# Optimization experiments

Measured on AMD Instinct MI355X. Metric: run time of the kernel, lower is better.

The kernel has to match this reference:

```python
import jax, jax.numpy as jnp
import numpy as np

N = 50000          # nodes
E = 800000         # edges (before self loops)
G = 64             # graphs in batch
HEADS = 4
HID = 25
DENSE = HEADS * HID      # 100, must equal prototype feature dim
IN_DIM = 128
OUT_DIM = 2
NPC = 5                  # num_prototypes_per_class
NUM_PROT = OUT_DIM * NPC
EPS = 1e-4
NEG_SLOPE = 0.2


def setup_inputs() -> dict:
    key = jax.random.key(0)
    ks = jax.random.split(key, 20)
    x = jax.random.normal(ks[0], (N, IN_DIM), dtype=jnp.float32)
    edge_index = jax.random.randint(ks[1], (2, E), 0, N, dtype=jnp.int64)
    batch = jnp.sort(jax.random.randint(ks[2], (N,), 0, G, dtype=jnp.int64))
    inp = {"x": x, "edge_index": edge_index, "batch": batch}
    in_dims = [IN_DIM, DENSE, DENSE]
    for i in range(3):
        d = in_dims[i]
        s = 1.0 / np.sqrt(d)
        inp[f"W{i}"] = jax.random.uniform(ks[3 + 4 * i], (d, DENSE), jnp.float32, -s, s)
        inp[f"as{i}"] = jax.random.uniform(ks[4 + 4 * i], (HEADS, HID), jnp.float32, -s, s)
        inp[f"ad{i}"] = jax.random.uniform(ks[5 + 4 * i], (HEADS, HID), jnp.float32, -s, s)
        inp[f"b{i}"] = jnp.zeros((DENSE,), jnp.float32)
    inp["protos"] = jax.random.uniform(ks[16], (NUM_PROT, DENSE), jnp.float32)
    # last_layer weight: +1 for own class, -0.5 otherwise  [OUT_DIM, NUM_PROT]
    cls = jnp.arange(NUM_PROT) // NPC
    inp["last_w"] = jnp.where(cls[None, :] == jnp.arange(OUT_DIM)[:, None], 1.0, -0.5).astype(jnp.float32)
    return inp


def _gat_layer(x, src, dst, W, a_src, a_dst, b):
    h = (x @ W).reshape(N, HEADS, HID)                 # [N,H,D]
    e_src = jnp.einsum('nhd,hd->nh', h, a_src)         # [N,H]
    e_dst = jnp.einsum('nhd,hd->nh', h, a_dst)
    alpha = e_src[src] + e_dst[dst]                    # [Etot,H]
    alpha = jnp.where(alpha > 0, alpha, NEG_SLOPE * alpha)
    amax = jax.ops.segment_max(alpha, dst, num_segments=N)
    ex = jnp.exp(alpha - amax[dst])
    denom = jax.ops.segment_sum(ex, dst, num_segments=N)
    a = ex / (denom[dst] + 1e-16)                      # segmented softmax over in-edges
    msg = h[src] * a[:, :, None]                       # [Etot,H,D]
    out = jax.ops.segment_sum(msg, dst, num_segments=N)
    return out.reshape(N, DENSE) + b


def reference(x, edge_index, batch, W0, as0, ad0, b0, W1, as1, ad1, b1, W2, as2, ad2, b2, protos, last_w):
    loops = jnp.arange(N, dtype=edge_index.dtype)
    src = jnp.concatenate([edge_index[0], loops])      # PyG add_self_loops=True
    dst = jnp.concatenate([edge_index[1], loops])
    params = [(W0, as0, ad0, b0), (W1, as1, ad1, b1), (W2, as2, ad2, b2)]
    h = x
    for (W, a_s, a_d, b) in params:
        h = _gat_layer(h, src, dst, W, a_s, a_d, b)
        h = jax.nn.relu(h)
    node_emb = h
    graph_emb = jax.ops.segment_max(h, batch, num_segments=G)   # global_max_pool
    # prototype distances: squared euclidean via expansion
    xp = graph_emb @ protos.T                                    # [G,P]
    dist = -2.0 * xp + jnp.sum(graph_emb ** 2, axis=1, keepdims=True) + jnp.sum(protos ** 2, axis=1)[None, :]
    sim = jnp.log((dist + 1.0) / (dist + EPS))
    logits = sim @ last_w.T
    probs = jax.nn.softmax(logits, axis=-1)
    return logits, probs, node_emb, graph_emb, dist
```

## Files before the change

kernel.cpp:

```cpp
#include <hip/hip_runtime.h>
#include <hip/hip_bf16.h>

#define NN      50000
#define EE      800000
#define ETOT    (EE + NN)
#define GG      64
#define HEADS   4
#define HID     25
#define DENSE   100
#define IN_DIM  128
#define OUT_DIM 2
#define NPC     5
#define NUM_PROT (OUT_DIM * NPC)
#define NCHUNK  ((NN + 255) / 256)

#define NEG_INF (-3.402823466e38f)

__global__ void k_count(const int* __restrict__ ei, int* __restrict__ cnt, int* __restrict__ pos) {
    int e = blockIdx.x * blockDim.x + threadIdx.x;
    if (e >= ETOT) return;
    int dst = (e < EE) ? ei[EE + e] : (e - EE);
    pos[e] = atomicAdd(&cnt[dst], 1);
}

__global__ void k_scan1(const int* __restrict__ cnt, int* __restrict__ csum) {
    __shared__ int sh[256];
    int i = blockIdx.x * 256 + threadIdx.x;
    int v = (i < NN) ? cnt[i] : 0;
    sh[threadIdx.x] = v;
    __syncthreads();
    for (int s = 128; s > 0; s >>= 1) {
        if (threadIdx.x < s) sh[threadIdx.x] += sh[threadIdx.x + s];
        __syncthreads();
    }
    if (threadIdx.x == 0) csum[blockIdx.x] = sh[0];
}

__global__ void k_scan2(int* __restrict__ csum) {
    __shared__ int sh[256];
    int tid = threadIdx.x;
    int v = (tid < NCHUNK) ? csum[tid] : 0;
    sh[tid] = v;
    __syncthreads();
    for (int s = 1; s < 256; s <<= 1) {
        int t = (tid >= s) ? sh[tid - s] : 0;
        __syncthreads();
        sh[tid] += t;
        __syncthreads();
    }
    if (tid < NCHUNK) csum[tid] = sh[tid] - v;
    if (tid == NCHUNK) csum[NCHUNK] = sh[255];
}

__global__ void k_scan3(const int* __restrict__ cnt, const int* __restrict__ csum, int* __restrict__ offs) {
    __shared__ int sh[256];
    int i = blockIdx.x * 256 + threadIdx.x;
    int v = (i < NN) ? cnt[i] : 0;
    sh[threadIdx.x] = v;
    __syncthreads();
    for (int s = 1; s < 256; s <<= 1) {
        int t = (threadIdx.x >= s) ? sh[threadIdx.x - s] : 0;
        __syncthreads();
        sh[threadIdx.x] += t;
        __syncthreads();
    }
    int excl = sh[threadIdx.x] - v + csum[blockIdx.x];
    if (i <= NN) offs[i] = excl;
}

__global__ void k_scatter(const int* __restrict__ ei, const int* __restrict__ offs,
                          const int* __restrict__ pos, int* __restrict__ csr) {
    int e = blockIdx.x * blockDim.x + threadIdx.x;
    if (e >= ETOT) return;
    int src, dst;
    if (e < EE) { src = ei[e]; dst = ei[EE + e]; }
    else        { src = dst = e - EE; }
    csr[offs[dst] + pos[e]] = src;
}

__global__ void k_bounds(const int* __restrict__ batch, int* __restrict__ gstart) {
    int n = blockIdx.x * blockDim.x + threadIdx.x;
    if (n >= NN) return;
    int b = batch[n];
    if (n == 0) {
        for (int g = 0; g <= b; g++) gstart[g] = 0;
    } else {
        int pb = batch[n - 1];
        for (int g = pb + 1; g <= b; g++) gstart[g] = n;
    }
    if (n == NN - 1) {
        for (int g = b + 1; g <= GG; g++) gstart[g] = NN;
    }
}

template <int DIN, int KC>
__global__ __launch_bounds__(256) void k_gemm(const float* __restrict__ X,
                                              const float* __restrict__ W,
                                              float* __restrict__ H) {
    constexpr int XSTR = KC + 4;
    __shared__ float Ws[KC * 104];
    __shared__ float Xs[128 * XSTR];
    const int tid = threadIdx.x;
    const int rl = tid >> 5;
    const int cg = tid & 31;
    const int node0 = blockIdx.x * 128;

    float acc[16][4] = {};
    constexpr int NCH = DIN / KC;
    constexpr int KQ = KC / 4;
    for (int kb = 0; kb < NCH; ++kb) {
        const int k0 = kb * KC;
        for (int idx = tid; idx < KC * 100; idx += 256) {
            int k = idx / 100, c = idx - k * 100;
            Ws[k * 104 + c] = W[(k0 + k) * 100 + c];
        }
        for (int q = tid; q < 128 * KQ; q += 256) {
            int r = q / KQ, kq = q - r * KQ;
            int row = node0 + r;
            float4 v = {0.f, 0.f, 0.f, 0.f};
            if (row < NN) v = *reinterpret_cast<const float4*>(&X[(size_t)row * DIN + k0 + kq * 4]);
            *reinterpret_cast<float4*>(&Xs[r * XSTR + kq * 4]) = v;
        }
        __syncthreads();
        if (cg < 25) {
            for (int kq = 0; kq < KQ; ++kq) {
                float4 w0 = *reinterpret_cast<const float4*>(&Ws[(kq * 4 + 0) * 104 + cg * 4]);
                float4 w1 = *reinterpret_cast<const float4*>(&Ws[(kq * 4 + 1) * 104 + cg * 4]);
                float4 w2 = *reinterpret_cast<const float4*>(&Ws[(kq * 4 + 2) * 104 + cg * 4]);
                float4 w3 = *reinterpret_cast<const float4*>(&Ws[(kq * 4 + 3) * 104 + cg * 4]);
                #pragma unroll
                for (int j = 0; j < 16; ++j) {
                    float4 xv = *reinterpret_cast<const float4*>(&Xs[(rl * 16 + j) * XSTR + kq * 4]);
                    acc[j][0] += xv.x * w0.x; acc[j][1] += xv.x * w0.y;
                    acc[j][2] += xv.x * w0.z; acc[j][3] += xv.x * w0.w;
                    acc[j][0] += xv.y * w1.x; acc[j][1] += xv.y * w1.y;
                    acc[j][2] += xv.y * w1.z; acc[j][3] += xv.y * w1.w;
                    acc[j][0] += xv.z * w2.x; acc[j][1] += xv.z * w2.y;
                    acc[j][2] += xv.z * w2.z; acc[j][3] += xv.z * w2.w;
                    acc[j][0] += xv.w * w3.x; acc[j][1] += xv.w * w3.y;
                    acc[j][2] += xv.w * w3.z; acc[j][3] += xv.w * w3.w;
                }
            }
        }
        __syncthreads();
    }
    if (cg < 25) {
        #pragma unroll
        for (int j = 0; j < 16; ++j) {
            int row = node0 + rl * 16 + j;
            if (row < NN) {
                float4 v = {acc[j][0], acc[j][1], acc[j][2], acc[j][3]};
                *reinterpret_cast<float4*>(&H[(size_t)row * 100 + cg * 4]) = v;
            }
        }
    }
}

__global__ void k_esed(const float* __restrict__ H, const float* __restrict__ AS,
                       const float* __restrict__ AD, float* __restrict__ es, float* __restrict__ ed) {
    int t = blockIdx.x * blockDim.x + threadIdx.x;
    if (t >= NN * HEADS) return;
    int n = t >> 2, hd = t & 3;
    const float* hr = H + (size_t)n * 100 + hd * 25;
    const float* as = AS + hd * 25;
    const float* ad = AD + hd * 25;
    float s1 = 0.f, s2 = 0.f;
    #pragma unroll
    for (int d = 0; d < 25; d++) {
        float v = hr[d];
        s1 += v * as[d];
        s2 += v * ad[d];
    }
    es[t] = s1;
    ed[t] = s2;
}

__global__ __launch_bounds__(256) void k_msum(const float* __restrict__ es,
                                              const float* __restrict__ ed,
                                              const int* __restrict__ offs,
                                              const int* __restrict__ csr,
                                              float* __restrict__ wv) {
    int wid = threadIdx.x >> 6;
    int lane = threadIdx.x & 63;
    int n = blockIdx.x * 4 + wid;
    if (n >= NN) return;
    int el = lane >> 2, hd = lane & 3;
    int beg = offs[n], end = offs[n + 1];
    float edh = ed[n * 4 + hd];
    float m = NEG_INF, s = 0.f;
    for (int e = beg + el; e < end; e += 16) {
        int si = csr[e];
        float a = es[si * 4 + hd] + edh;
        a = (a > 0.f) ? a : 0.2f * a;
        float nm = fmaxf(m, a);
        float sc = __expf(m - nm);
        s = s * sc + __expf(a - nm);
        m = nm;
    }
    #pragma unroll
    for (int mask = 4; mask <= 32; mask <<= 1) {
        float mo = __shfl_xor(m, mask, 64);
        float so = __shfl_xor(s, mask, 64);
        float nm = fmaxf(m, mo);
        float f1 = (m  > NEG_INF) ? __expf(m  - nm) : 0.f;
        float f2 = (mo > NEG_INF) ? __expf(mo - nm) : 0.f;
        s = s * f1 + so * f2;
        m = nm;
    }
    float invs = 1.f / (s + 1e-16f);
    for (int e = beg + el; e < end; e += 16) {
        int si = csr[e];
        float a = es[si * 4 + hd] + edh;
        a = (a > 0.f) ? a : 0.2f * a;
        wv[(size_t)e * 4 + hd] = __expf(a - m) * invs;
    }
}

__global__ __launch_bounds__(128) void k_acc(const float* __restrict__ H,
                                             const float* __restrict__ wv,
                                             const int* __restrict__ offs,
                                             const int* __restrict__ csr,
                                             const float* __restrict__ bias,
                                             float* __restrict__ out) {
    int wid = threadIdx.x >> 6;
    int lane = threadIdx.x & 63;
    int n = blockIdx.x * 2 + wid;
    if (n >= NN || lane >= 50) return;
    int d0 = lane * 2;
    int h0 = d0 / 25, h1 = (d0 + 1) / 25;
    int beg = offs[n], end = offs[n + 1];
    float ax = 0.f, ay = 0.f;
    for (int e = beg; e < end; e += 8) {
        #pragma unroll
        for (int u = 0; u < 8; ++u) {
            int ee = e + u;
            int ec = (ee < end) ? ee : beg;
            int idx = csr[ec];
            float wx = wv[(size_t)ec * 4 + h0];
            float wy = wv[(size_t)ec * 4 + h1];
            if (ee >= end) { wx = 0.f; wy = 0.f; }
            float2 xv = *reinterpret_cast<const float2*>(&H[(size_t)idx * 100 + d0]);
            ax += wx * xv.x;
            ay += wy * xv.y;
        }
    }
    float2 b = *reinterpret_cast<const float2*>(&bias[d0]);
    float2 o = {fmaxf(ax + b.x, 0.f), fmaxf(ay + b.y, 0.f)};
    *reinterpret_cast<float2*>(&out[(size_t)n * 100 + d0]) = o;
}

__global__ void k_pool1(const float* __restrict__ NE, const int* __restrict__ gstart,
                        float* __restrict__ part) {
    int g = blockIdx.x >> 3, c = blockIdx.x & 7;
    int d = threadIdx.x;
    if (d >= 100) return;
    int s0 = gstart[g], s1 = gstart[g + 1];
    int len = s1 - s0;
    int n0 = s0 + (int)((long long)len * c / 8);
    int n1 = s0 + (int)((long long)len * (c + 1) / 8);
    float vm = NEG_INF;
    for (int n = n0; n < n1; n++) vm = fmaxf(vm, NE[(size_t)n * 100 + d]);
    part[(size_t)(g * 8 + c) * 100 + d] = vm;
}

__global__ void k_pool2(const float* __restrict__ part, float* __restrict__ GE) {
    int g = blockIdx.x;
    int d = threadIdx.x;
    if (d >= 100) return;
    float vm = NEG_INF;
    for (int c = 0; c < 8; c++) vm = fmaxf(vm, part[(size_t)(g * 8 + c) * 100 + d]);
    GE[(size_t)g * 100 + d] = vm;
}

__global__ void k_head(const float* __restrict__ GE, const float* __restrict__ P,
                       const float* __restrict__ LW, float* __restrict__ logits,
                       float* __restrict__ probs, float* __restrict__ dist) {
    int g = blockIdx.x;
    __shared__ float ge[100];
    __shared__ float sims[NUM_PROT];
    __shared__ float lg[OUT_DIM];
    int t = threadIdx.x;
    if (t < 100) ge[t] = GE[(size_t)g * 100 + t];
    __syncthreads();
    if (t < NUM_PROT) {
        float dot = 0.f, pn = 0.f, gn = 0.f;
        for (int d = 0; d < 100; d++) {
            float pv = P[t * 100 + d];
            float gv = ge[d];
            dot += gv * pv;
            pn += pv * pv;
            gn += gv * gv;
        }
        float ds = gn - 2.f * dot + pn;
        dist[g * NUM_PROT + t] = ds;
        sims[t] = logf((ds + 1.f) / (ds + 1e-4f));
    }
    __syncthreads();
    if (t < OUT_DIM) {
        float l = 0.f;
        for (int p = 0; p < NUM_PROT; p++) l += sims[p] * LW[t * NUM_PROT + p];
        lg[t] = l;
        logits[g * OUT_DIM + t] = l;
    }
    __syncthreads();
    if (t == 0) {
        float mm = fmaxf(lg[0], lg[1]);
        float e0 = __expf(lg[0] - mm), e1 = __expf(lg[1] - mm);
        float inv = 1.f / (e0 + e1);
        probs[g * OUT_DIM + 0] = e0 * inv;
        probs[g * OUT_DIM + 1] = e1 * inv;
    }
}

extern "C" void kernel_launch(void* const* d_in, const int* in_sizes, int n_in,
                              void* d_out, int out_size, void* d_ws, size_t ws_size,
                              hipStream_t stream) {
    const float* x     = (const float*)d_in[0];
    const int*   ei    = (const int*)d_in[1];
    const int*   batch = (const int*)d_in[2];
    const float* Wm[3]  = {(const float*)d_in[3],  (const float*)d_in[7],  (const float*)d_in[11]};
    const float* ASm[3] = {(const float*)d_in[4],  (const float*)d_in[8],  (const float*)d_in[12]};
    const float* ADm[3] = {(const float*)d_in[5],  (const float*)d_in[9],  (const float*)d_in[13]};
    const float* Bm[3]  = {(const float*)d_in[6],  (const float*)d_in[10], (const float*)d_in[14]};
    const float* P  = (const float*)d_in[15];
    const float* LW = (const float*)d_in[16];

    float* out = (float*)d_out;
    float* logits  = out;
    float* probs   = out + GG * OUT_DIM;
    float* nodeEmb = out + 2 * GG * OUT_DIM;
    float* GE      = nodeEmb + (size_t)NN * DENSE;
    float* disto   = GE + GG * DENSE;

    char* w = (char*)d_ws;
    size_t off = 0;
    auto carve = [&](size_t bytes) -> void* {
        void* p = w + off;
        off += (bytes + 15) & ~(size_t)15;
        return p;
    };
    float* hA   = (float*)carve((size_t)NN * DENSE * 4);
    float* es   = (float*)carve((size_t)NN * HEADS * 4);
    float* ed   = (float*)carve((size_t)NN * HEADS * 4);
    int* cnt    = (int*)carve((size_t)NN * 4);
    int* offs   = (int*)carve((size_t)(NN + 1) * 4);
    int* pos    = (int*)carve((size_t)ETOT * 4);
    int* csr    = (int*)carve((size_t)ETOT * 4);
    int* csum   = (int*)carve((size_t)(NCHUNK + 1) * 4);
    int* gstart = (int*)carve((size_t)(GG + 1) * 4);
    float* part = (float*)carve((size_t)GG * 8 * DENSE * 4);
    float* wv   = (float*)carve((size_t)ETOT * HEADS * 4);
    (void)in_sizes; (void)n_in; (void)out_size; (void)ws_size;

    hipMemsetAsync(cnt, 0, (size_t)NN * 4, stream);
    k_count<<<(ETOT + 255) / 256, 256, 0, stream>>>(ei, cnt, pos);
    k_scan1<<<NCHUNK, 256, 0, stream>>>(cnt, csum);
    k_scan2<<<1, 256, 0, stream>>>(csum);
    k_scan3<<<NCHUNK, 256, 0, stream>>>(cnt, csum, offs);
    k_scatter<<<(ETOT + 255) / 256, 256, 0, stream>>>(ei, offs, pos, csr);
    k_bounds<<<(NN + 255) / 256, 256, 0, stream>>>(batch, gstart);

    const int gemmGrid = (NN + 127) / 128;
    const int esedGrid = (NN * HEADS + 255) / 256;
    const int msumGrid = (NN + 3) / 4;
    const int accGrid  = (NN + 1) / 2;

    const float* layerIn = x;
    for (int l = 0; l < 3; ++l) {
        if (l == 0) k_gemm<IN_DIM, 32><<<gemmGrid, 256, 0, stream>>>(layerIn, Wm[l], hA);
        else        k_gemm<DENSE,  20><<<gemmGrid, 256, 0, stream>>>(layerIn, Wm[l], hA);
        k_esed<<<esedGrid, 256, 0, stream>>>(hA, ASm[l], ADm[l], es, ed);
        k_msum<<<msumGrid, 256, 0, stream>>>(es, ed, offs, csr, wv);
        k_acc<<<accGrid, 128, 0, stream>>>(hA, wv, offs, csr, Bm[l], nodeEmb);
        layerIn = nodeEmb;
    }

    k_pool1<<<GG * 8, 128, 0, stream>>>(nodeEmb, gstart, part);
    k_pool2<<<GG, 128, 0, stream>>>(part, GE);

    k_head<<<GG, 128, 0, stream>>>(GE, P, LW, logits, probs, disto);
}
```

Before: 457.7 us.

## Fuse softmax normalization and message aggregation into one attention kernel

Merges the per-node softmax statistics kernel and the weighted-gather kernel into a single wavefront-per-node kernel. The edge weights are recomputed from es/ed inside the aggregation loop, so the per-edge weight buffer (ETOT x 4 floats) is no longer written and read back, and one launch per layer goes away. The aggregation now handles two edges per iteration, one per half-wave, each lane loading a float4 of features, with a shuffle reduction at the end. The cost is recomputing exp per edge for each feature lane, and only 50 of the 64 lanes do useful work.

```diff
diff --git a/kernel.cpp b/kernel.cpp
--- a/kernel.cpp
+++ b/kernel.cpp
@@ -175,78 +175,104 @@
     ed[t] = s2;
 }
 
-__global__ __launch_bounds__(256) void k_msum(const float* __restrict__ es,
+__global__ __launch_bounds__(256) void k_attn(const float* __restrict__ H,
+                                              const float* __restrict__ es,
                                               const float* __restrict__ ed,
                                               const int* __restrict__ offs,
                                               const int* __restrict__ csr,
-                                              float* __restrict__ wv) {
-    int wid = threadIdx.x >> 6;
-    int lane = threadIdx.x & 63;
-    int n = blockIdx.x * 4 + wid;
+                                              const float* __restrict__ bias,
+                                              float* __restrict__ out) {
+    const int wid = threadIdx.x >> 6;
+    const int lane = threadIdx.x & 63;
+    const int n = blockIdx.x * 4 + wid;
     if (n >= NN) return;
-    int el = lane >> 2, hd = lane & 3;
-    int beg = offs[n], end = offs[n + 1];
-    float edh = ed[n * 4 + hd];
-    float m = NEG_INF, s = 0.f;
-    for (int e = beg + el; e < end; e += 16) {
-        int si = csr[e];
-        float a = es[si * 4 + hd] + edh;
-        a = (a > 0.f) ? a : 0.2f * a;
-        float nm = fmaxf(m, a);
-        float sc = __expf(m - nm);
-        s = s * sc + __expf(a - nm);
-        m = nm;
-    }
-    #pragma unroll
-    for (int mask = 4; mask <= 32; mask <<= 1) {
-        float mo = __shfl_xor(m, mask, 64);
-        float so = __shfl_xor(s, mask, 64);
-        float nm = fmaxf(m, mo);
-        float f1 = (m  > NEG_INF) ? __expf(m  - nm) : 0.f;
-        float f2 = (mo > NEG_INF) ? __expf(mo - nm) : 0.f;
-        s = s * f1 + so * f2;
-        m = nm;
-    }
-    float invs = 1.f / (s + 1e-16f);
-    for (int e = beg + el; e < end; e += 16) {
-        int si = csr[e];
-        float a = es[si * 4 + hd] + edh;
-        a = (a > 0.f) ? a : 0.2f * a;
-        wv[(size_t)e * 4 + hd] = __expf(a - m) * invs;
-    }
-}
-
-__global__ __launch_bounds__(128) void k_acc(const float* __restrict__ H,
-                                             const float* __restrict__ wv,
-                                             const int* __restrict__ offs,
-                                             const int* __restrict__ csr,
-                                             const float* __restrict__ bias,
-                                             float* __restrict__ out) {
-    int wid = threadIdx.x >> 6;
-    int lane = threadIdx.x & 63;
-    int n = blockIdx.x * 2 + wid;
-    if (n >= NN || lane >= 50) return;
-    int d0 = lane * 2;
-    int h0 = d0 / 25, h1 = (d0 + 1) / 25;
-    int beg = offs[n], end = offs[n + 1];
-    float ax = 0.f, ay = 0.f;
-    for (int e = beg; e < end; e += 8) {
+    const int beg = offs[n], end = offs[n + 1];
+
+    {
+        const int el = lane >> 2, hd = lane & 3;
+        float edh = ed[n * 4 + hd];
+        float m = NEG_INF, s = 0.f;
+        for (int e = beg + el; e < end; e += 16) {
+            int si = csr[e];
+            float a = es[si * 4 + hd] + edh;
+            a = fmaxf(a, 0.2f * a);
+            float nm = fmaxf(m, a);
+            float sc = __expf(m - nm);
+            s = s * sc + __expf(a - nm);
+            m = nm;
+        }
         #pragma unroll
-        for (int u = 0; u < 8; ++u) {
-            int ee = e + u;
-            int ec = (ee < end) ? ee : beg;
-            int idx = csr[ec];
-            float wx = wv[(size_t)ec * 4 + h0];
-            float wy = wv[(size_t)ec * 4 + h1];
-            if (ee >= end) { wx = 0.f; wy = 0.f; }
-            float2 xv = *reinterpret_cast<const float2*>(&H[(size_t)idx * 100 + d0]);
-            ax += wx * xv.x;
-            ay += wy * xv.y;
-        }
-    }
-    float2 b = *reinterpret_cast<const float2*>(&bias[d0]);
-    float2 o = {fmaxf(ax + b.x, 0.f), fmaxf(ay + b.y, 0.f)};
-    *reinterpret_cast<float2*>(&out[(size_t)n * 100 + d0]) = o;
+        for (int mask = 4; mask <= 32; mask <<= 1) {
+            float mo = __shfl_xor(m, mask, 64);
+            float so = __shfl_xor(s, mask, 64);
+            float nm = fmaxf(m, mo);
+            float f1 = (m  > NEG_INF) ? __expf(m  - nm) : 0.f;
+            float f2 = (mo > NEG_INF) ? __expf(mo - nm) : 0.f;
+            s = s * f1 + so * f2;
+            m = nm;
+        }
+        float m0 = __shfl(m, 0, 64), m1 = __shfl(m, 1, 64);
+        float m2 = __shfl(m, 2, 64), m3 = __shfl(m, 3, 64);
+        float s0 = __shfl(s, 0, 64), s1 = __shfl(s, 1, 64);
+        float s2 = __shfl(s, 2, 64), s3 = __shfl(s, 3, 64);
+
+        const int h2 = lane >> 5;
+        const int q  = lane & 31;
+        const int d0 = q * 4;
+        const bool act = (q < 25);
+        const int hdA = d0 / 25;
+        const int hdB = (d0 + 3) / 25;
+        const bool selA1 = ((d0 + 1) / 25) == hdA;
+        const bool selA2 = ((d0 + 2) / 25) == hdA;
+        float4 ed4 = *reinterpret_cast<const float4*>(&ed[n * 4]);
+        auto pick = [&](int h, float v0, float v1, float v2, float v3) {
+            return h == 0 ? v0 : (h == 1 ? v1 : (h == 2 ? v2 : v3));
+        };
+        const float edA = pick(hdA, ed4.x, ed4.y, ed4.z, ed4.w);
+        const float edB = pick(hdB, ed4.x, ed4.y, ed4.z, ed4.w);
+        const float mA  = pick(hdA, m0, m1, m2, m3);
+        const float mB  = pick(hdB, m0, m1, m2, m3);
+        const float iA  = 1.f / (pick(hdA, s0, s1, s2, s3) + 1e-16f);
+        const float iB  = 1.f / (pick(hdB, s0, s1, s2, s3) + 1e-16f);
+
+        float ax = 0.f, ay = 0.f, az = 0.f, aw = 0.f;
+        for (int e0 = beg; e0 < end; e0 += 8) {
+            #pragma unroll
+            for (int u = 0; u < 4; ++u) {
+                int ee = e0 + u * 2 + h2;
+                bool valid = (ee < end);
+                int ec = valid ? ee : beg;
+                int si = csr[ec];
+                float4 e4 = *reinterpret_cast<const float4*>(&es[si * 4]);
+                float eAv = pick(hdA, e4.x, e4.y, e4.z, e4.w);
+                float eBv = pick(hdB, e4.x, e4.y, e4.z, e4.w);
+                float aA = eAv + edA; aA = fmaxf(aA, 0.2f * aA);
+                float aB = eBv + edB; aB = fmaxf(aB, 0.2f * aB);
+                float wA = __expf(aA - mA) * iA;
+                float wB = __expf(aB - mB) * iB;
+                if (!valid) { wA = 0.f; wB = 0.f; }
+                float w1 = selA1 ? wA : wB;
+                float w2 = selA2 ? wA : wB;
+                if (act) {
+                    float4 xv = *reinterpret_cast<const float4*>(&H[(size_t)si * 100 + d0]);
+                    ax += wA * xv.x;
+                    ay += w1 * xv.y;
+                    az += w2 * xv.z;
+                    aw += wB * xv.w;
+                }
+            }
+        }
+        ax += __shfl_xor(ax, 32, 64);
+        ay += __shfl_xor(ay, 32, 64);
+        az += __shfl_xor(az, 32, 64);
+        aw += __shfl_xor(aw, 32, 64);
+        if (act && h2 == 0) {
+            float4 b = *reinterpret_cast<const float4*>(&bias[d0]);
+            float4 o = {fmaxf(ax + b.x, 0.f), fmaxf(ay + b.y, 0.f),
+                        fmaxf(az + b.z, 0.f), fmaxf(aw + b.w, 0.f)};
+            *reinterpret_cast<float4*>(&out[(size_t)n * 100 + d0]) = o;
+        }
+    }
 }
 
 __global__ void k_pool1(const float* __restrict__ NE, const int* __restrict__ gstart,
@@ -349,7 +375,6 @@
     int* csum   = (int*)carve((size_t)(NCHUNK + 1) * 4);
     int* gstart = (int*)carve((size_t)(GG + 1) * 4);
     float* part = (float*)carve((size_t)GG * 8 * DENSE * 4);
-    float* wv   = (float*)carve((size_t)ETOT * HEADS * 4);
     (void)in_sizes; (void)n_in; (void)out_size; (void)ws_size;
 
     hipMemsetAsync(cnt, 0, (size_t)NN * 4, stream);
@@ -362,16 +387,14 @@
 
     const int gemmGrid = (NN + 127) / 128;
     const int esedGrid = (NN * HEADS + 255) / 256;
-    const int msumGrid = (NN + 3) / 4;
-    const int accGrid  = (NN + 1) / 2;
+    const int attnGrid = (NN + 3) / 4;
 
     const float* layerIn = x;
     for (int l = 0; l < 3; ++l) {
         if (l == 0) k_gemm<IN_DIM, 32><<<gemmGrid, 256, 0, stream>>>(layerIn, Wm[l], hA);
         else        k_gemm<DENSE,  20><<<gemmGrid, 256, 0, stream>>>(layerIn, Wm[l], hA);
         k_esed<<<esedGrid, 256, 0, stream>>>(hA, ASm[l], ADm[l], es, ed);
-        k_msum<<<msumGrid, 256, 0, stream>>>(es, ed, offs, csr, wv);
-        k_acc<<<accGrid, 128, 0, stream>>>(hA, wv, offs, csr, Bm[l], nodeEmb);
+        k_attn<<<attnGrid, 256, 0, stream>>>(hA, es, ed, offs, csr, Bm[l], nodeEmb);
         layerIn = nodeEmb;
     }
 
```

Result: slower. 521.8 us (+14.0%).

## Restructure node GEMM to stage full W in LDS and read X rows directly

Applied to the files above, without the earlier changes.

The GEMM now loads the whole weight matrix into shared memory once per block and has each wavefront handle 16 rows, with each lane computing two output columns. X rows are read directly from global memory as wavefront-uniform broadcast loads, dropping the X shared-memory tile and the per-chunk barriers. Blocks cover 64 rows instead of 128, so there are more blocks. Separately, 64-bit index casts in the aggregation kernel become 32-bit int arithmetic to cut address math. The risk is less data reuse per thread (2 columns instead of 4) and more global load instructions for X.

```diff
diff --git a/kernel.cpp b/kernel.cpp
--- a/kernel.cpp
+++ b/kernel.cpp
@@ -93,64 +93,65 @@
     }
 }
 
-template <int DIN, int KC>
+template <int DIN>
 __global__ __launch_bounds__(256) void k_gemm(const float* __restrict__ X,
                                               const float* __restrict__ W,
                                               float* __restrict__ H) {
-    constexpr int XSTR = KC + 4;
-    __shared__ float Ws[KC * 104];
-    __shared__ float Xs[128 * XSTR];
+    __shared__ float Ws[DIN * 102];
     const int tid = threadIdx.x;
-    const int rl = tid >> 5;
-    const int cg = tid & 31;
-    const int node0 = blockIdx.x * 128;
-
-    float acc[16][4] = {};
-    constexpr int NCH = DIN / KC;
-    constexpr int KQ = KC / 4;
-    for (int kb = 0; kb < NCH; ++kb) {
-        const int k0 = kb * KC;
-        for (int idx = tid; idx < KC * 100; idx += 256) {
-            int k = idx / 100, c = idx - k * 100;
-            Ws[k * 104 + c] = W[(k0 + k) * 100 + c];
-        }
-        for (int q = tid; q < 128 * KQ; q += 256) {
-            int r = q / KQ, kq = q - r * KQ;
-            int row = node0 + r;
-            float4 v = {0.f, 0.f, 0.f, 0.f};
-            if (row < NN) v = *reinterpret_cast<const float4*>(&X[(size_t)row * DIN + k0 + kq * 4]);
-            *reinterpret_cast<float4*>(&Xs[r * XSTR + kq * 4]) = v;
-        }
-        __syncthreads();
-        if (cg < 25) {
-            for (int kq = 0; kq < KQ; ++kq) {
-                float4 w0 = *reinterpret_cast<const float4*>(&Ws[(kq * 4 + 0) * 104 + cg * 4]);
-                float4 w1 = *reinterpret_cast<const float4*>(&Ws[(kq * 4 + 1) * 104 + cg * 4]);
-                float4 w2 = *reinterpret_cast<const float4*>(&Ws[(kq * 4 + 2) * 104 + cg * 4]);
-                float4 w3 = *reinterpret_cast<const float4*>(&Ws[(kq * 4 + 3) * 104 + cg * 4]);
-                #pragma unroll
-                for (int j = 0; j < 16; ++j) {
-                    float4 xv = *reinterpret_cast<const float4*>(&Xs[(rl * 16 + j) * XSTR + kq * 4]);
-                    acc[j][0] += xv.x * w0.x; acc[j][1] += xv.x * w0.y;
-                    acc[j][2] += xv.x * w0.z; acc[j][3] += xv.x * w0.w;
-                    acc[j][0] += xv.y * w1.x; acc[j][1] += xv.y * w1.y;
-                    acc[j][2] += xv.y * w1.z; acc[j][3] += xv.y * w1.w;
-                    acc[j][0] += xv.z * w2.x; acc[j][1] += xv.z * w2.y;
-                    acc[j][2] += xv.z * w2.z; acc[j][3] += xv.z * w2.w;
-                    acc[j][0] += xv.w * w3.x; acc[j][1] += xv.w * w3.y;
-                    acc[j][2] += xv.w * w3.z; acc[j][3] += xv.w * w3.w;
-                }
+    for (int idx = tid; idx < DIN * 100; idx += 256) {
+        int k = idx / 100, c = idx - k * 100;
+        Ws[k * 102 + c] = W[idx];
+    }
+    __syncthreads();
+
+    const int wv = tid >> 6;
+    const int lane = tid & 63;
+    const int row0 = blockIdx.x * 64 + wv * 16;
+    const int c0 = lane * 2;
+    const bool act = (lane < 50);
+
+    float accx[16], accy[16];
+    #pragma unroll
+    for (int r = 0; r < 16; ++r) { accx[r] = 0.f; accy[r] = 0.f; }
+
+    for (int kq = 0; kq < DIN / 4; ++kq) {
+        const int k0 = kq * 4;
+        float2 wk0, wk1, wk2, wk3;
+        if (act) {
+            wk0 = *reinterpret_cast<const float2*>(&Ws[(k0 + 0) * 102 + c0]);
+            wk1 = *reinterpret_cast<const float2*>(&Ws[(k0 + 1) * 102 + c0]);
+            wk2 = *reinterpret_cast<const float2*>(&Ws[(k0 + 2) * 102 + c0]);
+            wk3 = *reinterpret_cast<const float2*>(&Ws[(k0 + 3) * 102 + c0]);
+        } else {
+            wk0 = wk1 = wk2 = wk3 = float2{0.f, 0.f};
+        }
+        #pragma unroll
+        for (int h = 0; h < 2; ++h) {
+            float4 xv[8];
+            #pragma unroll
+            for (int r = 0; r < 8; ++r) {
+                int row = row0 + h * 8 + r;
+                int rc = (row < NN) ? row : (NN - 1);
+                xv[r] = *reinterpret_cast<const float4*>(&X[(size_t)rc * DIN + k0]);
             }
-        }
-        __syncthreads();
-    }
-    if (cg < 25) {
+            #pragma unroll
+            for (int r = 0; r < 8; ++r) {
+                int ar = h * 8 + r;
+                accx[ar] += xv[r].x * wk0.x; accy[ar] += xv[r].x * wk0.y;
+                accx[ar] += xv[r].y * wk1.x; accy[ar] += xv[r].y * wk1.y;
+                accx[ar] += xv[r].z * wk2.x; accy[ar] += xv[r].z * wk2.y;
+                accx[ar] += xv[r].w * wk3.x; accy[ar] += xv[r].w * wk3.y;
+            }
+        }
+    }
+    if (act) {
         #pragma unroll
-        for (int j = 0; j < 16; ++j) {
-            int row = node0 + rl * 16 + j;
+        for (int r = 0; r < 16; ++r) {
+            int row = row0 + r;
             if (row < NN) {
-                float4 v = {acc[j][0], acc[j][1], acc[j][2], acc[j][3]};
-                *reinterpret_cast<float4*>(&H[(size_t)row * 100 + cg * 4]) = v;
+                float2 v = {accx[r], accy[r]};
+                *reinterpret_cast<float2*>(&H[(size_t)row * 100 + c0]) = v;
             }
         }
     }
@@ -236,17 +237,17 @@
             int ee = e + u;
             int ec = (ee < end) ? ee : beg;
             int idx = csr[ec];
-            float wx = wv[(size_t)ec * 4 + h0];
-            float wy = wv[(size_t)ec * 4 + h1];
+            float wx = wv[ec * 4 + h0];
+            float wy = wv[ec * 4 + h1];
             if (ee >= end) { wx = 0.f; wy = 0.f; }
-            float2 xv = *reinterpret_cast<const float2*>(&H[(size_t)idx * 100 + d0]);
+            float2 xv = *reinterpret_cast<const float2*>(&H[idx * 100 + d0]);
             ax += wx * xv.x;
             ay += wy * xv.y;
         }
     }
     float2 b = *reinterpret_cast<const float2*>(&bias[d0]);
     float2 o = {fmaxf(ax + b.x, 0.f), fmaxf(ay + b.y, 0.f)};
-    *reinterpret_cast<float2*>(&out[(size_t)n * 100 + d0]) = o;
+    *reinterpret_cast<float2*>(&out[n * 100 + d0]) = o;
 }
 
 __global__ void k_pool1(const float* __restrict__ NE, const int* __restrict__ gstart,
@@ -360,15 +361,15 @@
     k_scatter<<<(ETOT + 255) / 256, 256, 0, stream>>>(ei, offs, pos, csr);
     k_bounds<<<(NN + 255) / 256, 256, 0, stream>>>(batch, gstart);
 
-    const int gemmGrid = (NN + 127) / 128;
+    const int gemmGrid = (NN + 63) / 64;
     const int esedGrid = (NN * HEADS + 255) / 256;
     const int msumGrid = (NN + 3) / 4;
     const int accGrid  = (NN + 1) / 2;
 
     const float* layerIn = x;
     for (int l = 0; l < 3; ++l) {
-        if (l == 0) k_gemm<IN_DIM, 32><<<gemmGrid, 256, 0, stream>>>(layerIn, Wm[l], hA);
-        else        k_gemm<DENSE,  20><<<gemmGrid, 256, 0, stream>>>(layerIn, Wm[l], hA);
+        if (l == 0) k_gemm<IN_DIM><<<gemmGrid, 256, 0, stream>>>(layerIn, Wm[l], hA);
+        else        k_gemm<DENSE ><<<gemmGrid, 256, 0, stream>>>(layerIn, Wm[l], hA);
         k_esed<<<esedGrid, 256, 0, stream>>>(hA, ASm[l], ADm[l], es, ed);
         k_msum<<<msumGrid, 256, 0, stream>>>(es, ed, offs, csr, wv);
         k_acc<<<accGrid, 128, 0, stream>>>(hA, wv, offs, csr, Bm[l], nodeEmb);
```

Measured after the change: 532.7 us. 1.16x slower.

## Retile GEMM to 8x8 register blocks with transposed shared-memory X

Applied to the files above, without the earlier changes.

The node GEMM kernel switches from 16x4 per-thread tiles over 25 active column groups to an 8x8 outer-product tile across all 256 threads. X is now stored transposed in shared memory and W is padded to 128 columns in groups of 12, so each k step needs only four vector LDS loads. This is meant to raise FMA-to-LDS-load ratio and keep all threads busy, at the cost of some wasted compute on padded columns. Separately, the aggregation kernel uses 32-bit index arithmetic instead of size_t to save address computation.

```diff
diff --git a/kernel.cpp b/kernel.cpp
--- a/kernel.cpp
+++ b/kernel.cpp
@@ -97,60 +97,68 @@
 __global__ __launch_bounds__(256) void k_gemm(const float* __restrict__ X,
                                               const float* __restrict__ W,
                                               float* __restrict__ H) {
-    constexpr int XSTR = KC + 4;
-    __shared__ float Ws[KC * 104];
-    __shared__ float Xs[128 * XSTR];
+    constexpr int NCH = DIN / KC;
+    constexpr int KQ  = KC / 4;
+    constexpr int XP  = 132;
+    constexpr int WP  = 192;
+    __shared__ float Xs[KC * XP];
+    __shared__ float Ws[KC * WP];
     const int tid = threadIdx.x;
-    const int rl = tid >> 5;
-    const int cg = tid & 31;
+    const int tr = tid >> 4;
+    const int tc = tid & 15;
     const int node0 = blockIdx.x * 128;
 
-    float acc[16][4] = {};
-    constexpr int NCH = DIN / KC;
-    constexpr int KQ = KC / 4;
-    for (int kb = 0; kb < NCH; ++kb) {
-        const int k0 = kb * KC;
-        for (int idx = tid; idx < KC * 100; idx += 256) {
-            int k = idx / 100, c = idx - k * 100;
-            Ws[k * 104 + c] = W[(k0 + k) * 100 + c];
-        }
-        for (int q = tid; q < 128 * KQ; q += 256) {
-            int r = q / KQ, kq = q - r * KQ;
-            int row = node0 + r;
+    float acc[8][8] = {};
+    for (int ch = 0; ch < NCH; ++ch) {
+        const int k0 = ch * KC;
+        for (int idx = tid; idx < 128 * KQ; idx += 256) {
+            int row = idx / KQ, kq = idx - row * KQ;
+            int gr = node0 + row;
             float4 v = {0.f, 0.f, 0.f, 0.f};
-            if (row < NN) v = *reinterpret_cast<const float4*>(&X[(size_t)row * DIN + k0 + kq * 4]);
-            *reinterpret_cast<float4*>(&Xs[r * XSTR + kq * 4]) = v;
-        }
-        __syncthreads();
-        if (cg < 25) {
-            for (int kq = 0; kq < KQ; ++kq) {
-                float4 w0 = *reinterpret_cast<const float4*>(&Ws[(kq * 4 + 0) * 104 + cg * 4]);
-                float4 w1 = *reinterpret_cast<const float4*>(&Ws[(kq * 4 + 1) * 104 + cg * 4]);
-                float4 w2 = *reinterpret_cast<const float4*>(&Ws[(kq * 4 + 2) * 104 + cg * 4]);
-                float4 w3 = *reinterpret_cast<const float4*>(&Ws[(kq * 4 + 3) * 104 + cg * 4]);
+            if (gr < NN) v = *reinterpret_cast<const float4*>(&X[(size_t)gr * DIN + k0 + kq * 4]);
+            Xs[(kq * 4 + 0) * XP + row] = v.x;
+            Xs[(kq * 4 + 1) * XP + row] = v.y;
+            Xs[(kq * 4 + 2) * XP + row] = v.z;
+            Xs[(kq * 4 + 3) * XP + row] = v.w;
+        }
+        for (int idx = tid; idx < KC * 128; idx += 256) {
+            int k = idx >> 7, c = idx & 127;
+            int g = c >> 3, j = c & 7;
+            float v = (c < 100) ? W[(size_t)(k0 + k) * 100 + c] : 0.f;
+            Ws[k * WP + g * 12 + j] = v;
+        }
+        __syncthreads();
+        #pragma unroll 4
+        for (int k = 0; k < KC; ++k) {
+            float4 xa = *reinterpret_cast<const float4*>(&Xs[k * XP + tr * 8]);
+            float4 xb = *reinterpret_cast<const float4*>(&Xs[k * XP + tr * 8 + 4]);
+            float4 wa = *reinterpret_cast<const float4*>(&Ws[k * WP + tc * 12]);
+            float4 wb = *reinterpret_cast<const float4*>(&Ws[k * WP + tc * 12 + 4]);
+            float xs[8] = {xa.x, xa.y, xa.z, xa.w, xb.x, xb.y, xb.z, xb.w};
+            float ws[8] = {wa.x, wa.y, wa.z, wa.w, wb.x, wb.y, wb.z, wb.w};
+            #pragma unroll
+            for (int r = 0; r < 8; ++r) {
                 #pragma unroll
-                for (int j = 0; j < 16; ++j) {
-                    float4 xv = *reinterpret_cast<const float4*>(&Xs[(rl * 16 + j) * XSTR + kq * 4]);
-                    acc[j][0] += xv.x * w0.x; acc[j][1] += xv.x * w0.y;
-                    acc[j][2] += xv.x * w0.z; acc[j][3] += xv.x * w0.w;
-                    acc[j][0] += xv.y * w1.x; acc[j][1] += xv.y * w1.y;
-                    acc[j][2] += xv.y * w1.z; acc[j][3] += xv.y * w1.w;
-                    acc[j][0] += xv.z * w2.x; acc[j][1] += xv.z * w2.y;
-                    acc[j][2] += xv.z * w2.z; acc[j][3] += xv.z * w2.w;
-                    acc[j][0] += xv.w * w3.x; acc[j][1] += xv.w * w3.y;
-                    acc[j][2] += xv.w * w3.z; acc[j][3] += xv.w * w3.w;
+                for (int c = 0; c < 8; ++c) {
+                    acc[r][c] += xs[r] * ws[c];
                 }
             }
         }
         __syncthreads();
     }
-    if (cg < 25) {
+    const int c0 = tc * 8;
+    if (c0 < 100) {
         #pragma unroll
-        for (int j = 0; j < 16; ++j) {
-            int row = node0 + rl * 16 + j;
+        for (int r = 0; r < 8; ++r) {
+            int row = node0 + tr * 8 + r;
             if (row < NN) {
-                float4 v = {acc[j][0], acc[j][1], acc[j][2], acc[j][3]};
-                *reinterpret_cast<float4*>(&H[(size_t)row * 100 + cg * 4]) = v;
+                float* hp = &H[(size_t)row * 100 + c0];
+                float4 v0 = {acc[r][0], acc[r][1], acc[r][2], acc[r][3]};
+                *reinterpret_cast<float4*>(hp) = v0;
+                if (c0 + 4 < 100) {
+                    float4 v1 = {acc[r][4], acc[r][5], acc[r][6], acc[r][7]};
+                    *reinterpret_cast<float4*>(hp + 4) = v1;
+                }
             }
         }
     }
@@ -236,17 +244,17 @@
             int ee = e + u;
             int ec = (ee < end) ? ee : beg;
             int idx = csr[ec];
-            float wx = wv[(size_t)ec * 4 + h0];
-            float wy = wv[(size_t)ec * 4 + h1];
+            float wx = wv[ec * 4 + h0];
+            float wy = wv[ec * 4 + h1];
             if (ee >= end) { wx = 0.f; wy = 0.f; }
-            float2 xv = *reinterpret_cast<const float2*>(&H[(size_t)idx * 100 + d0]);
+            float2 xv = *reinterpret_cast<const float2*>(&H[idx * 100 + d0]);
             ax += wx * xv.x;
             ay += wy * xv.y;
         }
     }
     float2 b = *reinterpret_cast<const float2*>(&bias[d0]);
     float2 o = {fmaxf(ax + b.x, 0.f), fmaxf(ay + b.y, 0.f)};
-    *reinterpret_cast<float2*>(&out[(size_t)n * 100 + d0]) = o;
+    *reinterpret_cast<float2*>(&out[n * 100 + d0]) = o;
 }
 
 __global__ void k_pool1(const float* __restrict__ NE, const int* __restrict__ gstart,
```

Measured after the change: 462.9 us. No clear change (+1.1%).
